# Performance work log

Hardware: AMD Instinct MI355X
Metric: run time of the kernel (lower is better)

The kernel has to match this reference:

```python
import jax, jax.numpy as jnp
import numpy as np

B, N, L = 1, 128, 256
D_MSA, D_HID, D_PAIR = 256, 32, 128
EPS = 1e-5


def setup_inputs() -> dict:
    key = jax.random.key(0)
    ks = jax.random.split(key, 8)
    msa = jax.random.normal(ks[0], (B, N, L, D_MSA), dtype=jnp.float32)
    pair = jax.random.normal(ks[1], (B, L, L, D_PAIR), dtype=jnp.float32)
    symmids = jax.random.randint(ks[2], (1,), 0, 1, dtype=jnp.int64)
    symmsub = jax.random.randint(ks[3], (1,), 0, 1, dtype=jnp.int64)
    # learned params (lecun-normal-ish scale = 1/sqrt(fan_in))
    ln_gamma = jnp.ones((D_MSA,), jnp.float32)
    ln_beta = jnp.zeros((D_MSA,), jnp.float32)
    w_left = jax.random.normal(ks[4], (D_MSA, D_HID), jnp.float32) / np.sqrt(D_MSA)
    b_left = jnp.zeros((D_HID,), jnp.float32)
    w_right = jax.random.normal(ks[5], (D_MSA, D_HID), jnp.float32) / np.sqrt(D_MSA)
    b_right = jnp.zeros((D_HID,), jnp.float32)
    w_out = jax.random.normal(ks[6], (D_HID * D_HID, D_PAIR), jnp.float32) / np.sqrt(D_HID * D_HID)
    b_out = jnp.zeros((D_PAIR,), jnp.float32)
    return {
        "msa": msa, "pair": pair, "symmids": symmids, "symmsub": symmsub,
        "ln_gamma": ln_gamma, "ln_beta": ln_beta,
        "w_left": w_left, "b_left": b_left,
        "w_right": w_right, "b_right": b_right,
        "w_out": w_out, "b_out": b_out,
    }


def reference(msa, pair, symmids, symmsub, ln_gamma, ln_beta,
              w_left, b_left, w_right, b_right, w_out, b_out):
    b, n, l, _ = msa.shape
    # LayerNorm over d_msa (biased variance, matching torch)
    mu = jnp.mean(msa, axis=-1, keepdims=True)
    var = jnp.mean(jnp.square(msa - mu), axis=-1, keepdims=True)
    x = (msa - mu) * jax.lax.rsqrt(var + EPS) * ln_gamma + ln_beta
    left = x @ w_left + b_left                       # [b, n, l, d_h]
    right = (x @ w_right + b_right) / float(n)       # [b, n, l, d_h]
    # outer product, reduced over MSA (s) dim -> [b, l, m, d_h, d_h]
    out = jnp.einsum('bsli,bsmj->blmij', left, right).reshape(b, l, l, -1)
    out = out @ w_out + b_out                        # [b, l, l, d_pair]
    return pair + out
```

## Files before the change

kernel.cpp:

```cpp
#include <hip/hip_runtime.h>


typedef float v4f __attribute__((ext_vector_type(4)));
typedef short v8s __attribute__((ext_vector_type(8)));

static __device__ inline unsigned short f2bf(float x) {
    unsigned int u = __builtin_bit_cast(unsigned int, x);
    return (unsigned short)((u + 0x7fffu + ((u >> 16) & 1u)) >> 16);
}

static __device__ inline void gl_lds16(const unsigned short* g, unsigned short* l) {
    __builtin_amdgcn_global_load_lds(
        (const __attribute__((address_space(1))) unsigned int*)g,
        (__attribute__((address_space(3))) unsigned int*)(unsigned long long)l,
        16, 0, 0);
}

__global__ __launch_bounds__(256) void k_prep(const float* __restrict__ w_out,
                                              const float* __restrict__ wl,
                                              const float* __restrict__ wr,
                                              unsigned short* __restrict__ w3,
                                              unsigned short* __restrict__ wB) {
    const int b = blockIdx.x, t = threadIdx.x;
    unsigned short tmp[8];
    if (b < 64) {
        int tgt = b * 2048 + t * 8;
        int lane6 = (tgt >> 3) & 63, quad = lane6 >> 4, l15 = lane6 & 15;
        int w = (tgt >> 9) & 7;
        int inner = (tgt >> 12) & 1, ck = tgt >> 13;
        int p = w * 16 + l15;
        for (int e = 0; e < 8; ++e) {
            int kp = ck * 64 + inner * 32 + quad * 8 + e;
            int j1 = (kp >> 9) & 1, qd = (kp >> 7) & 3, lp = (kp >> 3) & 15;
            int i1 = (kp >> 2) & 1, r = kp & 3;
            int ii = i1 * 16 + qd * 4 + r, jj = j1 * 16 + lp;
            tmp[e] = f2bf(w_out[(ii * 32 + jj) * 128 + p]);
        }
        *(uint4*)&w3[tgt] = *(const uint4*)tmp;
    } else {
        int tgt = (b - 64) * 2048 + t * 8;
        int frag = tgt >> 9, lane6 = (tgt >> 3) & 63;
        int nt = frag >> 3, ks = frag & 7;
        int quad = lane6 >> 4, l15 = lane6 & 15;
        int c = nt * 16 + l15;
        const float* src = (c < 32) ? wl : wr;
        int cc = c & 31;
        for (int e = 0; e < 8; ++e) {
            int d = ks * 32 + quad * 8 + e;
            tmp[e] = f2bf(src[d * 32 + cc]);
        }
        *(uint4*)&wB[tgt] = *(const uint4*)tmp;
    }
}

__global__ __launch_bounds__(256) void k_lnproj(
    const float* __restrict__ msa, const float* __restrict__ gamma, const float* __restrict__ beta,
    const unsigned short* __restrict__ wB, const float* __restrict__ bl, const float* __restrict__ br,
    unsigned short* __restrict__ leftT, unsigned short* __restrict__ rightT) {
    __shared__ unsigned short xb[32 * 264];
    __shared__ unsigned short outT[64 * 40];

    const int t = threadIdx.x, lane = t & 63, w = t >> 6;
    const int l = blockIdx.x, s0 = blockIdx.y * 32;
    const int quad = lane >> 4, l15 = lane & 15;

    float4 g4 = *(const float4*)&gamma[lane * 4];
    float4 be4 = *(const float4*)&beta[lane * 4];
    float4 vr[8]; float s1[8], s2[8];
    for (int r = 0; r < 8; ++r) {
        const float* row = msa + (size_t)((s0 + w * 8 + r) * 256 + l) * 256;
        vr[r] = *(const float4*)&row[lane * 4];
    }
    for (int r = 0; r < 8; ++r) {
        float4 v = vr[r];
        s1[r] = v.x + v.y + v.z + v.w;
        s2[r] = v.x * v.x + v.y * v.y + v.z * v.z + v.w * v.w;
    }
    for (int o = 32; o > 0; o >>= 1)
        for (int r = 0; r < 8; ++r) { s1[r] += __shfl_xor(s1[r], o); s2[r] += __shfl_xor(s2[r], o); }
    for (int r = 0; r < 8; ++r) {
        float mu = s1[r] * (1.f / 256);
        float rs = rsqrtf(s2[r] * (1.f / 256) - mu * mu + 1e-5f);
        float4 v = vr[r];
        ushort4 xs;
        xs.x = f2bf((v.x - mu) * rs * g4.x + be4.x);
        xs.y = f2bf((v.y - mu) * rs * g4.y + be4.y);
        xs.z = f2bf((v.z - mu) * rs * g4.z + be4.z);
        xs.w = f2bf((v.w - mu) * rs * g4.w + be4.w);
        *(ushort4*)&xb[(w * 8 + r) * 264 + lane * 4] = xs;
    }
    __syncthreads();

    const int mt = w >> 1, ntb = (w & 1) * 2;
    v4f acc[2] = {};
    const int frow = (mt * 16 + l15) * 264;
    const unsigned short* wBp = wB + lane * 8;
#pragma unroll
    for (int ks = 0; ks < 8; ++ks) {
        v8s a = *(const v8s*)&xb[frow + ks * 32 + quad * 8];
        v8s b0 = *(const v8s*)&wBp[(ntb * 8 + ks) * 512];
        v8s b1 = *(const v8s*)&wBp[((ntb + 1) * 8 + ks) * 512];
        acc[0] = __builtin_amdgcn_mfma_f32_16x16x32_bf16(a, b0, acc[0], 0, 0, 0);
        acc[1] = __builtin_amdgcn_mfma_f32_16x16x32_bf16(a, b1, acc[1], 0, 0, 0);
    }

    for (int tn = 0; tn < 2; ++tn) {
        int c = (ntb + tn) * 16 + l15;
        float bias = c < 32 ? bl[c] : br[c - 32];
        float scale = c < 32 ? 1.f : (1.f / 128);
        for (int r = 0; r < 4; ++r)
            outT[c * 40 + mt * 16 + quad * 4 + r] = f2bf((acc[tn][r] + bias) * scale);
    }
    __syncthreads();

    {
        int c = t >> 2, q = t & 3;
        uint4 vv = *(const uint4*)&outT[c * 40 + q * 8];
        int cc = c & 31;
        unsigned short* base = (c < 32) ? leftT : rightT;
        unsigned short* dst = base + l * 4096 + blockIdx.y * 1024
                            + (cc >> 4) * 512 + q * 128 + (cc & 15) * 8;
        *(uint4*)dst = vv;
    }
}

__global__ __launch_bounds__(512, 4) void k_outer(
    const unsigned short* __restrict__ leftT, const unsigned short* __restrict__ rightT,
    const unsigned short* __restrict__ w2g, const float* __restrict__ bout,
    const float* __restrict__ pairIn, float* __restrict__ out) {
    __shared__ alignas(16) unsigned short smem[32768];
    unsigned short* Ah = smem;
    unsigned short* Bh = smem + 16384;
    unsigned short* Obuf = smem;
    float* Pbuf = (float*)smem;

    const int t = threadIdx.x, lane = t & 63, w = t >> 6;
    const int l0 = blockIdx.x * 8, m0 = blockIdx.y * 4;
    const int wm = w & 3, wn = w >> 2;
    const int quad = lane >> 4, l15 = lane & 15;

    const unsigned short* Asrc = leftT + l0 * 4096;
    const unsigned short* Bsrc = rightT + m0 * 4096;

    v4f acc[4][4] = {};
    for (int kh = 0; kh < 2; ++kh) {
        if (kh) __syncthreads();
#pragma unroll
        for (int it = 0; it < 4; ++it) {
            int x = (it * 512 + t) * 8;
            gl_lds16(&Asrc[(x >> 11) * 4096 + kh * 2048 + (x & 2047)], &Ah[x]);
        }
#pragma unroll
        for (int it = 0; it < 2; ++it) {
            int x = (it * 512 + t) * 8;
            gl_lds16(&Bsrc[(x >> 11) * 4096 + kh * 2048 + (x & 2047)], &Bh[x]);
        }
        __syncthreads();
#pragma unroll
        for (int kl = 0; kl < 2; ++kl) {
            v8s a[4], bb[4];
#pragma unroll
            for (int i = 0; i < 4; ++i)
                a[i] = *(const v8s*)&Ah[(wm * 2 + (i >> 1)) * 2048 + kl * 1024 + (i & 1) * 512 + lane * 8];
#pragma unroll
            for (int j = 0; j < 4; ++j)
                bb[j] = *(const v8s*)&Bh[(wn * 2 + (j >> 1)) * 2048 + kl * 1024 + (j & 1) * 512 + lane * 8];
#pragma unroll
            for (int i = 0; i < 4; ++i)
#pragma unroll
                for (int j = 0; j < 4; ++j)
                    acc[i][j] = __builtin_amdgcn_mfma_f32_16x16x32_bf16(a[i], bb[j], acc[i][j], 0, 0, 0);
        }
    }
    __syncthreads();

    const unsigned short* wsrc = w2g + w * 512 + lane * 8;
    v8s A0 = *(const v8s*)&wsrc[0];
    v8s A1 = *(const v8s*)&wsrc[4096];
    v8s B0 = *(const v8s*)&wsrc[8192];
    v8s B1 = *(const v8s*)&wsrc[8192 + 4096];
    const int p = w * 16 + l15;
    float bo = bout[p];

    for (int a2 = 0; a2 < 2; ++a2)
        for (int b2 = 0; b2 < 2; ++b2) {
            int P = (wm * 2 + a2) * 4 + wn * 2 + b2;
            for (int j1 = 0; j1 < 2; ++j1) {
                unsigned short tmp8[8];
                for (int i1 = 0; i1 < 2; ++i1)
                    for (int r = 0; r < 4; ++r)
                        tmp8[i1 * 4 + r] = f2bf(acc[a2 * 2 + i1][b2 * 2 + j1][r]);
                int pg = (j1 * 64 + lane) ^ (P & 7) ^ ((P & 8) << 3);
                *(uint4*)&Obuf[P * 1024 + pg * 8] = *(const uint4*)tmp8;
            }
        }
    __syncthreads();

    v4f aI0[2] = {}, aI1[2] = {};
#pragma unroll
    for (int ck = 0; ck < 16; ck += 2) {
        {
            int g = ck * 8 + quad;
            int ch = ((g ^ (l15 & 7) ^ ((l15 & 8) << 3)) << 3);
            v8s a0 = *(const v8s*)&Obuf[l15 * 1024 + ch];
            v8s a1 = *(const v8s*)&Obuf[(16 + l15) * 1024 + ch];
            aI0[0] = __builtin_amdgcn_mfma_f32_16x16x32_bf16(a0, A0, aI0[0], 0, 0, 0);
            aI0[1] = __builtin_amdgcn_mfma_f32_16x16x32_bf16(a1, A0, aI0[1], 0, 0, 0);
            int g2 = ck * 8 + 4 + quad;
            int ch2 = ((g2 ^ (l15 & 7) ^ ((l15 & 8) << 3)) << 3);
            v8s b0 = *(const v8s*)&Obuf[l15 * 1024 + ch2];
            v8s b1 = *(const v8s*)&Obuf[(16 + l15) * 1024 + ch2];
            aI1[0] = __builtin_amdgcn_mfma_f32_16x16x32_bf16(b0, A1, aI1[0], 0, 0, 0);
            aI1[1] = __builtin_amdgcn_mfma_f32_16x16x32_bf16(b1, A1, aI1[1], 0, 0, 0);
            if (ck + 2 < 16) {
                const unsigned short* nx = wsrc + (ck + 2) * 8192;
                A0 = *(const v8s*)&nx[0];
                A1 = *(const v8s*)&nx[4096];
            }
        }
        {
            int g = (ck + 1) * 8 + quad;
            int ch = ((g ^ (l15 & 7) ^ ((l15 & 8) << 3)) << 3);
            v8s a0 = *(const v8s*)&Obuf[l15 * 1024 + ch];
            v8s a1 = *(const v8s*)&Obuf[(16 + l15) * 1024 + ch];
            aI0[0] = __builtin_amdgcn_mfma_f32_16x16x32_bf16(a0, B0, aI0[0], 0, 0, 0);
            aI0[1] = __builtin_amdgcn_mfma_f32_16x16x32_bf16(a1, B0, aI0[1], 0, 0, 0);
            int g2 = (ck + 1) * 8 + 4 + quad;
            int ch2 = ((g2 ^ (l15 & 7) ^ ((l15 & 8) << 3)) << 3);
            v8s b0 = *(const v8s*)&Obuf[l15 * 1024 + ch2];
            v8s b1 = *(const v8s*)&Obuf[(16 + l15) * 1024 + ch2];
            aI1[0] = __builtin_amdgcn_mfma_f32_16x16x32_bf16(b0, B1, aI1[0], 0, 0, 0);
            aI1[1] = __builtin_amdgcn_mfma_f32_16x16x32_bf16(b1, B1, aI1[1], 0, 0, 0);
            if (ck + 3 < 16) {
                const unsigned short* nx = wsrc + (ck + 3) * 8192;
                B0 = *(const v8s*)&nx[0];
                B1 = *(const v8s*)&nx[4096];
            }
        }
    }

    const float* psrc = pairIn + (size_t)((l0 + w) * 256 + m0) * 128 + lane * 2;
    float2 pp[4];
#pragma unroll
    for (int sub = 0; sub < 4; ++sub) pp[sub] = *(const float2*)&psrc[sub * 128];

    __syncthreads();

#pragma unroll
    for (int pm = 0; pm < 2; ++pm)
#pragma unroll
        for (int r = 0; r < 4; ++r) {
            int P = pm * 16 + quad * 4 + r;
            Pbuf[P * 132 + p] = (pm ? aI0[1][r] + aI1[1][r] : aI0[0][r] + aI1[0][r]) + bo;
        }
    __syncthreads();

    float* odst = out + (size_t)((l0 + w) * 256 + m0) * 128 + lane * 2;
#pragma unroll
    for (int sub = 0; sub < 4; ++sub) {
        int P = w * 4 + sub;
        float2 pv = *(const float2*)&Pbuf[P * 132 + lane * 2];
        float2 ov;
        ov.x = pp[sub].x + pv.x;
        ov.y = pp[sub].y + pv.y;
        *(float2*)&odst[sub * 128] = ov;
    }
}

extern "C" void kernel_launch(void* const* d_in, const int* in_sizes, int n_in,
                              void* d_out, int out_size, void* d_ws, size_t ws_size,
                              hipStream_t stream) {
    const float* msa   = (const float*)d_in[0];
    const float* pairI = (const float*)d_in[1];
    const float* gamma = (const float*)d_in[4];
    const float* beta  = (const float*)d_in[5];
    const float* wl    = (const float*)d_in[6];
    const float* bl    = (const float*)d_in[7];
    const float* wr    = (const float*)d_in[8];
    const float* br    = (const float*)d_in[9];
    const float* wout  = (const float*)d_in[10];
    const float* bout  = (const float*)d_in[11];
    float* out = (float*)d_out;

    unsigned short* leftT  = (unsigned short*)d_ws;
    unsigned short* rightT = leftT + 256 * 32 * 128;
    unsigned short* w3     = rightT + 256 * 32 * 128;
    unsigned short* wB     = w3 + 131072;

    k_prep<<<dim3(72), 256, 0, stream>>>(wout, wl, wr, w3, wB);
    k_lnproj<<<dim3(256, 4), 256, 0, stream>>>(msa, gamma, beta, wB, bl, br, leftT, rightT);
    k_outer<<<dim3(32, 64), 512, 0, stream>>>(leftT, rightT, w3, bout, pairI, out);
}
```

Baseline: 161.6 us.

## Use 32x32x16 MFMA with split-K across waves for the output projection

```diff
diff --git a/kernel.cpp b/kernel.cpp
--- a/kernel.cpp
+++ b/kernel.cpp
@@ -2,6 +2,7 @@
 
 
 typedef float v4f __attribute__((ext_vector_type(4)));
+typedef float f32x16 __attribute__((ext_vector_type(16)));
 typedef short v8s __attribute__((ext_vector_type(8)));
 
 static __device__ inline unsigned short f2bf(float x) {
@@ -19,24 +20,25 @@
 __global__ __launch_bounds__(256) void k_prep(const float* __restrict__ w_out,
                                               const float* __restrict__ wl,
                                               const float* __restrict__ wr,
-                                              unsigned short* __restrict__ w3,
+                                              unsigned short* __restrict__ w3n,
                                               unsigned short* __restrict__ wB) {
     const int b = blockIdx.x, t = threadIdx.x;
     unsigned short tmp[8];
     if (b < 64) {
         int tgt = b * 2048 + t * 8;
-        int lane6 = (tgt >> 3) & 63, quad = lane6 >> 4, l15 = lane6 & 15;
-        int w = (tgt >> 9) & 7;
-        int inner = (tgt >> 12) & 1, ck = tgt >> 13;
-        int p = w * 16 + l15;
+        int l = (tgt >> 3) & 63;
+        int pg = (tgt >> 9) & 3;
+        int kc = (tgt >> 11) & 31;
+        int kh = (tgt >> 16) & 1;
+        int p = pg * 32 + (l & 31);
         for (int e = 0; e < 8; ++e) {
-            int kp = ck * 64 + inner * 32 + quad * 8 + e;
+            int kp = kh * 512 + kc * 16 + (l >> 5) * 8 + e;
             int j1 = (kp >> 9) & 1, qd = (kp >> 7) & 3, lp = (kp >> 3) & 15;
             int i1 = (kp >> 2) & 1, r = kp & 3;
             int ii = i1 * 16 + qd * 4 + r, jj = j1 * 16 + lp;
             tmp[e] = f2bf(w_out[(ii * 32 + jj) * 128 + p]);
         }
-        *(uint4*)&w3[tgt] = *(const uint4*)tmp;
+        *(uint4*)&w3n[tgt] = *(const uint4*)tmp;
     } else {
         int tgt = (b - 64) * 2048 + t * 8;
         int frag = tgt >> 9, lane6 = (tgt >> 3) & 63;
@@ -128,11 +130,12 @@
     const unsigned short* __restrict__ leftT, const unsigned short* __restrict__ rightT,
     const unsigned short* __restrict__ w2g, const float* __restrict__ bout,
     const float* __restrict__ pairIn, float* __restrict__ out) {
-    __shared__ alignas(16) unsigned short smem[32768];
+    __shared__ alignas(16) unsigned short smem[40960];
     unsigned short* Ah = smem;
     unsigned short* Bh = smem + 16384;
     unsigned short* Obuf = smem;
     float* Pbuf = (float*)smem;
+    float* Rbuf = (float*)(smem + 32768);
 
     const int t = threadIdx.x, lane = t & 63, w = t >> 6;
     const int l0 = blockIdx.x * 8, m0 = blockIdx.y * 4;
@@ -174,13 +177,15 @@
     }
     __syncthreads();
 
-    const unsigned short* wsrc = w2g + w * 512 + lane * 8;
-    v8s A0 = *(const v8s*)&wsrc[0];
-    v8s A1 = *(const v8s*)&wsrc[4096];
-    v8s B0 = *(const v8s*)&wsrc[8192];
-    v8s B1 = *(const v8s*)&wsrc[8192 + 4096];
-    const int p = w * 16 + l15;
-    float bo = bout[p];
+    const int pg = w & 3, khB = w >> 2;
+    const int px = lane & 31, kB = lane >> 5;
+    const int swz = (px & 7) ^ ((px & 8) << 3);
+    const int gb = khB * 64 + kB;
+    const unsigned short* w3p = w2g + (khB * 32 * 4 + pg) * 512 + lane * 8;
+    v8s F0 = *(const v8s*)&w3p[0];
+    v8s F1 = *(const v8s*)&w3p[2048];
+    v8s F2 = *(const v8s*)&w3p[4096];
+    v8s F3 = *(const v8s*)&w3p[6144];
 
     for (int a2 = 0; a2 < 2; ++a2)
         for (int b2 = 0; b2 < 2; ++b2) {
@@ -190,53 +195,41 @@
                 for (int i1 = 0; i1 < 2; ++i1)
                     for (int r = 0; r < 4; ++r)
                         tmp8[i1 * 4 + r] = f2bf(acc[a2 * 2 + i1][b2 * 2 + j1][r]);
-                int pg = (j1 * 64 + lane) ^ (P & 7) ^ ((P & 8) << 3);
-                *(uint4*)&Obuf[P * 1024 + pg * 8] = *(const uint4*)tmp8;
+                int pgx = (j1 * 64 + lane) ^ (P & 7) ^ ((P & 8) << 3);
+                *(uint4*)&Obuf[P * 1024 + pgx * 8] = *(const uint4*)tmp8;
             }
         }
     __syncthreads();
 
-    v4f aI0[2] = {}, aI1[2] = {};
-#pragma unroll
-    for (int ck = 0; ck < 16; ck += 2) {
-        {
-            int g = ck * 8 + quad;
-            int ch = ((g ^ (l15 & 7) ^ ((l15 & 8) << 3)) << 3);
-            v8s a0 = *(const v8s*)&Obuf[l15 * 1024 + ch];
-            v8s a1 = *(const v8s*)&Obuf[(16 + l15) * 1024 + ch];
-            aI0[0] = __builtin_amdgcn_mfma_f32_16x16x32_bf16(a0, A0, aI0[0], 0, 0, 0);
-            aI0[1] = __builtin_amdgcn_mfma_f32_16x16x32_bf16(a1, A0, aI0[1], 0, 0, 0);
-            int g2 = ck * 8 + 4 + quad;
-            int ch2 = ((g2 ^ (l15 & 7) ^ ((l15 & 8) << 3)) << 3);
-            v8s b0 = *(const v8s*)&Obuf[l15 * 1024 + ch2];
-            v8s b1 = *(const v8s*)&Obuf[(16 + l15) * 1024 + ch2];
-            aI1[0] = __builtin_amdgcn_mfma_f32_16x16x32_bf16(b0, A1, aI1[0], 0, 0, 0);
-            aI1[1] = __builtin_amdgcn_mfma_f32_16x16x32_bf16(b1, A1, aI1[1], 0, 0, 0);
-            if (ck + 2 < 16) {
-                const unsigned short* nx = wsrc + (ck + 2) * 8192;
-                A0 = *(const v8s*)&nx[0];
-                A1 = *(const v8s*)&nx[4096];
-            }
-        }
-        {
-            int g = (ck + 1) * 8 + quad;
-            int ch = ((g ^ (l15 & 7) ^ ((l15 & 8) << 3)) << 3);
-            v8s a0 = *(const v8s*)&Obuf[l15 * 1024 + ch];
-            v8s a1 = *(const v8s*)&Obuf[(16 + l15) * 1024 + ch];
-            aI0[0] = __builtin_amdgcn_mfma_f32_16x16x32_bf16(a0, B0, aI0[0], 0, 0, 0);
-            aI0[1] = __builtin_amdgcn_mfma_f32_16x16x32_bf16(a1, B0, aI0[1], 0, 0, 0);
-            int g2 = (ck + 1) * 8 + 4 + quad;
-            int ch2 = ((g2 ^ (l15 & 7) ^ ((l15 & 8) << 3)) << 3);
-            v8s b0 = *(const v8s*)&Obuf[l15 * 1024 + ch2];
-            v8s b1 = *(const v8s*)&Obuf[(16 + l15) * 1024 + ch2];
-            aI1[0] = __builtin_amdgcn_mfma_f32_16x16x32_bf16(b0, B1, aI1[0], 0, 0, 0);
-            aI1[1] = __builtin_amdgcn_mfma_f32_16x16x32_bf16(b1, B1, aI1[1], 0, 0, 0);
-            if (ck + 3 < 16) {
-                const unsigned short* nx = wsrc + (ck + 3) * 8192;
-                B0 = *(const v8s*)&nx[0];
-                B1 = *(const v8s*)&nx[4096];
-            }
-        }
+    f32x16 ac0 = {}, ac1 = {};
+#pragma unroll
+    for (int o = 0; o < 8; ++o) {
+        {   int kc = o * 4;
+            v8s a = *(const v8s*)&Obuf[px * 1024 + (((gb + kc * 2) ^ swz) << 3)];
+            ac0 = __builtin_amdgcn_mfma_f32_32x32x16_bf16(a, F0, ac0, 0, 0, 0);
+            if (kc + 4 < 32) F0 = *(const v8s*)&w3p[(kc + 4) * 2048];
+        }
+        {   int kc = o * 4 + 1;
+            v8s a = *(const v8s*)&Obuf[px * 1024 + (((gb + kc * 2) ^ swz) << 3)];
+            ac1 = __builtin_amdgcn_mfma_f32_32x32x16_bf16(a, F1, ac1, 0, 0, 0);
+            if (kc + 4 < 32) F1 = *(const v8s*)&w3p[(kc + 4) * 2048];
+        }
+        {   int kc = o * 4 + 2;
+            v8s a = *(const v8s*)&Obuf[px * 1024 + (((gb + kc * 2) ^ swz) << 3)];
+            ac0 = __builtin_amdgcn_mfma_f32_32x32x16_bf16(a, F2, ac0, 0, 0, 0);
+            if (kc + 4 < 32) F2 = *(const v8s*)&w3p[(kc + 4) * 2048];
+        }
+        {   int kc = o * 4 + 3;
+            v8s a = *(const v8s*)&Obuf[px * 1024 + (((gb + kc * 2) ^ swz) << 3)];
+            ac1 = __builtin_amdgcn_mfma_f32_32x32x16_bf16(a, F3, ac1, 0, 0, 0);
+            if (kc + 4 < 32) F3 = *(const v8s*)&w3p[(kc + 4) * 2048];
+        }
+    }
+    f32x16 accB = ac0 + ac1;
+
+    if (khB == 1) {
+#pragma unroll
+        for (int s = 0; s < 16; ++s) Rbuf[s * 256 + pg * 64 + lane] = accB[s];
     }
 
     const float* psrc = pairIn + (size_t)((l0 + w) * 256 + m0) * 128 + lane * 2;
@@ -246,13 +239,15 @@
 
     __syncthreads();
 
-#pragma unroll
-    for (int pm = 0; pm < 2; ++pm)
-#pragma unroll
-        for (int r = 0; r < 4; ++r) {
-            int P = pm * 16 + quad * 4 + r;
-            Pbuf[P * 132 + p] = (pm ? aI0[1][r] + aI1[1][r] : aI0[0][r] + aI1[0][r]) + bo;
-        }
+    if (khB == 0) {
+        float bo = bout[pg * 32 + px];
+#pragma unroll
+        for (int s = 0; s < 16; ++s) {
+            float v = accB[s] + Rbuf[s * 256 + pg * 64 + lane] + bo;
+            int pxr = (s & 3) + 8 * (s >> 2) + 4 * kB;
+            Pbuf[pxr * 132 + pg * 32 + px] = v;
+        }
+    }
     __syncthreads();
 
     float* odst = out + (size_t)((l0 + w) * 256 + m0) * 128 + lane * 2;
@@ -284,10 +279,10 @@
 
     unsigned short* leftT  = (unsigned short*)d_ws;
     unsigned short* rightT = leftT + 256 * 32 * 128;
-    unsigned short* w3     = rightT + 256 * 32 * 128;
-    unsigned short* wB     = w3 + 131072;
-
-    k_prep<<<dim3(72), 256, 0, stream>>>(wout, wl, wr, w3, wB);
+    unsigned short* w3n    = rightT + 256 * 32 * 128;
+    unsigned short* wB     = w3n + 131072;
+
+    k_prep<<<dim3(72), 256, 0, stream>>>(wout, wl, wr, w3n, wB);
     k_lnproj<<<dim3(256, 4), 256, 0, stream>>>(msa, gamma, beta, wB, bl, br, leftT, rightT);
-    k_outer<<<dim3(32, 64), 512, 0, stream>>>(leftT, rightT, w3, bout, pairI, out);
-}
+    k_outer<<<dim3(32, 64), 512, 0, stream>>>(leftT, rightT, w3n, bout, pairI, out);
+}
```

Result: slower. 173.2 us (+7.2%).
